# Kernel tuning notes

Measured on AMD Instinct MI355X. Metric: run time of the kernel, lower is better.

The kernel has to match this reference:

```python
import math
import jax, jax.numpy as jnp
import numpy as np

B, N, D = 16384, 16, 2
HIDDEN, DL = 64, 5
OMEGA = 1.0
CUSP_GAMMA = 1.0 / (D - 1)  # dim=2 -> 1.0


def _linear_params(key, fan_in, fan_out):
    kw, kb = jax.random.split(key)
    bound = 1.0 / math.sqrt(fan_in)
    w = jax.random.uniform(kw, (fan_out, fan_in), jnp.float32, -bound, bound)
    b = jax.random.uniform(kb, (fan_out,), jnp.float32, -bound, bound)
    return w, b


def setup_inputs() -> dict:
    key = jax.random.key(0)
    ks = jax.random.split(key, 9)
    x = jax.random.normal(ks[0], (B, N, D), jnp.float32)
    phi_w0, phi_b0 = _linear_params(ks[1], D + 1, HIDDEN)
    phi_w1, phi_b1 = _linear_params(ks[2], HIDDEN, HIDDEN)
    phi_w2, phi_b2 = _linear_params(ks[3], HIDDEN, DL)
    psi_w0, psi_b0 = _linear_params(ks[4], 6, HIDDEN)
    psi_w1, psi_b1 = _linear_params(ks[5], HIDDEN, HIDDEN)
    psi_w2, psi_b2 = _linear_params(ks[6], HIDDEN, DL)
    rho_w0, rho_b0 = _linear_params(ks[7], 2 * DL, HIDDEN)
    # rho output layer: weight std=0.01 normal, bias zeros (matches torch init)
    rho_w1 = 0.01 * jax.random.normal(ks[8], (1, HIDDEN), jnp.float32)
    rho_b1 = jnp.zeros((1,), jnp.float32)
    return dict(x=x,
                phi_w0=phi_w0, phi_b0=phi_b0, phi_w1=phi_w1, phi_b1=phi_b1,
                phi_w2=phi_w2, phi_b2=phi_b2,
                psi_w0=psi_w0, psi_b0=psi_b0, psi_w1=psi_w1, psi_b1=psi_b1,
                psi_w2=psi_w2, psi_b2=psi_b2,
                rho_w0=rho_w0, rho_b0=rho_b0, rho_w1=rho_w1, rho_b1=rho_b1)


def _mlp3(h, w0, b0, w1, b1, w2, b2):
    h = jax.nn.gelu(h @ w0.T + b0, approximate=False)
    h = jax.nn.gelu(h @ w1.T + b1, approximate=False)
    return h @ w2.T + b2


def reference(x, phi_w0, phi_b0, phi_w1, phi_b1, phi_w2, phi_b2,
              psi_w0, psi_b0, psi_w1, psi_b1, psi_w2, psi_b2,
              rho_w0, rho_b0, rho_w1, rho_b1):
    # one-body branch
    xs = x * math.sqrt(OMEGA)                       # [B,N,D]
    r2 = (xs ** 2).sum(-1, keepdims=True)           # [B,N,1]
    phi_in = jnp.concatenate([xs, r2], -1)          # [B,N,D+1]
    phi_out = _mlp3(phi_in, phi_w0, phi_b0, phi_w1, phi_b1, phi_w2, phi_b2).mean(1)  # [B,dL]

    # two-body branch: vectorized over all N*(N-1)/2 pairs
    ii, jj = jnp.triu_indices(N, k=1)               # static pair index lists, P entries
    dr = x[:, ii, :] - x[:, jj, :]                  # [B,P,D]
    rij = jnp.sqrt((dr ** 2).sum(-1) + 1e-12)       # [B,P]
    feat = jnp.stack([jnp.log1p(rij), rij / (1 + rij), jnp.exp(-rij ** 2),
                      jnp.exp(-0.5 * rij), jnp.exp(-rij), jnp.exp(-2 * rij)], -1)  # [B,P,6]
    psi_out = _mlp3(feat, psi_w0, psi_b0, psi_w1, psi_b1, psi_w2, psi_b2).mean(1)  # [B,dL]
    cusp = CUSP_GAMMA * (rij * jnp.exp(-rij)).sum(-1)  # [B]

    # readout
    rho_in = jnp.concatenate([phi_out, psi_out], -1)   # [B,2*dL]
    h = jax.nn.gelu(rho_in @ rho_w0.T + rho_b0, approximate=False)
    f = (h @ rho_w1.T + rho_b1).squeeze(-1)            # [B]
    return f + cusp
```

## Files before the change

### kernel.cpp

```cpp
#include <hip/hip_runtime.h>
#include <hip/hip_bf16.h>
#include <math.h>

#define B_TOT 16384
#define NPART 16
#define NPAIR 120
#define HID   64
#define DL    5
#define GB    4
#define PSI_ROWS 120
#define PHI_HROW 120
#define NROW_IT  136
#define SF_PHI   480

typedef __attribute__((ext_vector_type(8))) short short8;
typedef __attribute__((ext_vector_type(4))) float floatx4;
typedef __attribute__((ext_vector_type(2))) unsigned uintx2;

#define CSC      2.45556851f
#define INV_CSC  0.40723744f

__device__ __forceinline__ float gelu_pre(float z) {
    float e = __builtin_amdgcn_exp2f(-z);
    return z * __builtin_amdgcn_rcpf(1.0f + e);
}

__device__ __forceinline__ float gelu_sig(float v) {
    float e = __builtin_amdgcn_exp2f(-2.45556851f * v);
    return v * __builtin_amdgcn_rcpf(1.0f + e);
}

__device__ __forceinline__ unsigned pk2(float a, float b) {
    __hip_bfloat162 h = __float22bfloat162_rn(make_float2(a, b));
    union { __hip_bfloat162 h; unsigned u; } cv; cv.h = h;
    return cv.u;
}

__device__ __forceinline__ float wred(float v) {
    v += __shfl_down(v, 32);
    v += __shfl_down(v, 16);
    v += __shfl_down(v, 8);
    v += __shfl_down(v, 4);
    v += __shfl_down(v, 2);
    v += __shfl_down(v, 1);
    return v;
}

__global__ __launch_bounds__(256) void jastrow_mfma12(
    const float* __restrict__ x,
    const float* __restrict__ phi_w0, const float* __restrict__ phi_b0,
    const float* __restrict__ phi_w1, const float* __restrict__ phi_b1,
    const float* __restrict__ phi_w2, const float* __restrict__ phi_b2,
    const float* __restrict__ psi_w0, const float* __restrict__ psi_b0,
    const float* __restrict__ psi_w1, const float* __restrict__ psi_b1,
    const float* __restrict__ psi_w2, const float* __restrict__ psi_b2,
    const float* __restrict__ rho_w0, const float* __restrict__ rho_b0,
    const float* __restrict__ rho_w1, const float* __restrict__ rho_b1,
    float* __restrict__ out)
{
    const int t    = threadIdx.x;
    const int lane = t & 63;
    const int wv   = t >> 6;
    const int q    = lane >> 4;
    const int m15  = lane & 15;
    const int bg   = blockIdx.x * GB;

    __shared__ __align__(16) unsigned short s_h[NROW_IT * 64];
    __shared__ __align__(16) unsigned char  s_mem[8704];
    __shared__ float s_cusp[GB];

    unsigned short* s_f  = (unsigned short*)s_mem;
    float*          s_cs = (float*)s_mem;

    const float2* x2 = (const float2*)x;
    float cusp = 0.f;

    {
        const int bl = wv;
        {
            int p = lane;
            int u = 119 - p;
            float sq = sqrtf((float)(8 * u + 1));
            int k = (int)((sq - 1.0f) * 0.5f);
            int i = 14 - k;
            int j = p - (i * (31 - i)) / 2 + i + 1;

            float2 xi = x2[(bg + bl) * NPART + i];
            float2 xj = x2[(bg + bl) * NPART + j];
            float dx = xi.x - xj.x, dy = xi.y - xj.y;
            float r = sqrtf(dx * dx + dy * dy + 1e-12f);

            float f0 = 0.69314718056f * __builtin_amdgcn_logf(1.f + r);
            float f1 = r * __builtin_amdgcn_rcpf(1.f + r);
            float f3 = __builtin_amdgcn_exp2f(-0.72134752044f * r);
            float f4 = f3 * f3;
            float f5 = f4 * f4;
            float f2 = __builtin_amdgcn_exp2f(-1.44269504089f * r * r);
            cusp += r * f4;

            union { short8 s; unsigned u4[4]; } v;
            v.u4[0] = pk2(f0, f1);
            v.u4[1] = pk2(f2, f3);
            v.u4[2] = pk2(f4, f5);
            v.u4[3] = 0u;
            *(short8*)&s_f[(bl * PSI_ROWS + p) * 8] = v.s;
        }
        if (lane < NPAIR - 64) {
            int p = 64 + lane;
            int u = 119 - p;
            float sq = sqrtf((float)(8 * u + 1));
            int k = (int)((sq - 1.0f) * 0.5f);
            int i = 14 - k;
            int j = p - (i * (31 - i)) / 2 + i + 1;

            float2 xi = x2[(bg + bl) * NPART + i];
            float2 xj = x2[(bg + bl) * NPART + j];
            float dx = xi.x - xj.x, dy = xi.y - xj.y;
            float r = sqrtf(dx * dx + dy * dy + 1e-12f);

            float f0 = 0.69314718056f * __builtin_amdgcn_logf(1.f + r);
            float f1 = r * __builtin_amdgcn_rcpf(1.f + r);
            float f3 = __builtin_amdgcn_exp2f(-0.72134752044f * r);
            float f4 = f3 * f3;
            float f5 = f4 * f4;
            float f2 = __builtin_amdgcn_exp2f(-1.44269504089f * r * r);
            cusp += r * f4;

            union { short8 s; unsigned u4[4]; } v;
            v.u4[0] = pk2(f0, f1);
            v.u4[1] = pk2(f2, f3);
            v.u4[2] = pk2(f4, f5);
            v.u4[3] = 0u;
            *(short8*)&s_f[(bl * PSI_ROWS + p) * 8] = v.s;
        }
        if (lane >= 48) {
            int n = lane - 48;
            float2 xv = x2[(bg + bl) * NPART + n];
            float r2 = xv.x * xv.x + xv.y * xv.y;
            union { short8 s; unsigned u4[4]; } w;
            w.u4[0] = pk2(xv.x, xv.y);
            w.u4[1] = pk2(r2, 0.f);
            w.u4[2] = 0u; w.u4[3] = 0u;
            *(short8*)&s_f[(SF_PHI + bl * NPART + n) * 8] = w.s;
        }
    }

    const int colb = wv * 16 + m15;

    short8 Ap1[4];
    floatx4 C0p4[4];
#pragma unroll
    for (int ht = 0; ht < 4; ++ht) {
        short8 f = (short8)0;
        if (q == 0) {
            const float* w = psi_w0 + (ht * 16 + m15) * 6;
            union { short8 s; unsigned u4[4]; } bb;
            bb.u4[0] = pk2(CSC * w[0], CSC * w[1]);
            bb.u4[1] = pk2(CSC * w[2], CSC * w[3]);
            bb.u4[2] = pk2(CSC * w[4], CSC * w[5]);
            bb.u4[3] = 0u;
            f = bb.s;
        }
        Ap1[ht] = f;
        floatx4 bv = *(const floatx4*)(psi_b0 + ht * 16 + q * 4);
        C0p4[ht] = bv * CSC;
    }
    short8 Af1 = (short8)0;
    if (q == 0) {
        const float* wf = phi_w0 + (wv * 16 + m15) * 3;
        union { short8 s; unsigned u4[4]; } bb;
        bb.u4[0] = pk2(CSC * wf[0], CSC * wf[1]);
        bb.u4[1] = pk2(CSC * wf[2], 0.f);
        bb.u4[2] = 0u; bb.u4[3] = 0u;
        Af1 = bb.s;
    }
    floatx4 C0fv = (*(const floatx4*)(phi_b0 + wv * 16 + q * 4)) * CSC;

    int scolw[4];
#pragma unroll
    for (int ht = 0; ht < 4; ++ht)
        scolw[ht] = (ht * 16 + q * 4) ^ ((m15 & 7) << 3);
    const int scolwp = (wv * 16 + q * 4) ^ ((m15 & 7) << 3);

    short8 Bp2[2], Bf2[2];
#pragma unroll
    for (int Kc = 0; Kc < 2; ++Kc) {
        const floatx4* wp4 = (const floatx4*)(psi_w1 + colb * HID + Kc * 32 + q * 8);
        const floatx4* wf4 = (const floatx4*)(phi_w1 + colb * HID + Kc * 32 + q * 8);
        floatx4 pA = wp4[0], pB = wp4[1];
        floatx4 fA = wf4[0], fB = wf4[1];
        union { short8 s; unsigned u4[4]; } bp, bf;
        bp.u4[0] = pk2(pA[0], pA[1]); bp.u4[1] = pk2(pA[2], pA[3]);
        bp.u4[2] = pk2(pB[0], pB[1]); bp.u4[3] = pk2(pB[2], pB[3]);
        bf.u4[0] = pk2(fA[0], fA[1]); bf.u4[1] = pk2(fA[2], fA[3]);
        bf.u4[2] = pk2(fB[0], fB[1]); bf.u4[3] = pk2(fB[2], fB[3]);
        Bp2[Kc] = bp.s; Bf2[Kc] = bf.s;
    }
    float b1p = CSC * psi_b1[colb], b1f = CSC * phi_b1[colb];
    floatx4 C1p = {b1p, b1p, b1p, b1p};
    floatx4 C1f = {b1f, b1f, b1f, b1f};

    const int g0 = ((q ^ (m15 & 7)) << 3);
    const int g1 = g0 ^ 32;

    float csP[GB] = {0.f, 0.f, 0.f, 0.f};
    float csF[GB] = {0.f, 0.f, 0.f, 0.f};

    __syncthreads();

#pragma unroll
    for (int bl = 0; bl < GB; ++bl) {
#pragma unroll
        for (int ti = 0; ti < 2; ++ti) {
            const int Mt = wv * 2 + ti;
            short8 b = *(const short8*)&s_f[(bl * PSI_ROWS + Mt * 16 + m15) * 8];
            unsigned short* wp = &s_h[(Mt * 16 + m15) * 64];
            const bool wr = (Mt != 7) || (m15 < 8);
#pragma unroll
            for (int ht = 0; ht < 4; ++ht) {
                floatx4 d = __builtin_amdgcn_mfma_f32_16x16x32_bf16(Ap1[ht], b, C0p4[ht], 0, 0, 0);
                unsigned u0 = pk2(gelu_pre(d[0]), gelu_pre(d[1]));
                unsigned u1 = pk2(gelu_pre(d[2]), gelu_pre(d[3]));
                if (wr) {
                    uintx2 v = {u0, u1};
                    *(uintx2*)(wp + scolw[ht]) = v;
                }
            }
        }
        {
            short8 b = *(const short8*)&s_f[(SF_PHI + bl * NPART + m15) * 8];
            unsigned short* wp = &s_h[(PHI_HROW + m15) * 64];
            floatx4 d = __builtin_amdgcn_mfma_f32_16x16x32_bf16(Af1, b, C0fv, 0, 0, 0);
            unsigned u0 = pk2(gelu_pre(d[0]), gelu_pre(d[1]));
            unsigned u1 = pk2(gelu_pre(d[2]), gelu_pre(d[3]));
            uintx2 v = {u0, u1};
            *(uintx2*)(wp + scolwp) = v;
        }
        __syncthreads();

#pragma unroll
        for (int Mt = 0; Mt < 8; ++Mt) {
            int rb = (Mt * 16 + m15) * 64;
            short8 a0 = *(const short8*)&s_h[rb + g0];
            short8 a1 = *(const short8*)&s_h[rb + g1];
            floatx4 acc = __builtin_amdgcn_mfma_f32_16x16x32_bf16(a0, Bp2[0], C1p, 0, 0, 0);
            acc = __builtin_amdgcn_mfma_f32_16x16x32_bf16(a1, Bp2[1], acc, 0, 0, 0);
            if (Mt == 7) {
                if (q < 2) {
#pragma unroll
                    for (int rg = 0; rg < 4; ++rg) {
                        float z = acc[rg];
                        float rr = __builtin_amdgcn_rcpf(1.0f + __builtin_amdgcn_exp2f(-z));
                        csP[bl] = __builtin_fmaf(z, rr, csP[bl]);
                    }
                }
            } else {
#pragma unroll
                for (int rg = 0; rg < 4; ++rg) {
                    float z = acc[rg];
                    float rr = __builtin_amdgcn_rcpf(1.0f + __builtin_amdgcn_exp2f(-z));
                    csP[bl] = __builtin_fmaf(z, rr, csP[bl]);
                }
            }
        }
        {
            int rb = (PHI_HROW + m15) * 64;
            short8 a0 = *(const short8*)&s_h[rb + g0];
            short8 a1 = *(const short8*)&s_h[rb + g1];
            floatx4 acc = __builtin_amdgcn_mfma_f32_16x16x32_bf16(a0, Bf2[0], C1f, 0, 0, 0);
            acc = __builtin_amdgcn_mfma_f32_16x16x32_bf16(a1, Bf2[1], acc, 0, 0, 0);
#pragma unroll
            for (int rg = 0; rg < 4; ++rg) {
                float z = acc[rg];
                float rr = __builtin_amdgcn_rcpf(1.0f + __builtin_amdgcn_exp2f(-z));
                csF[bl] = __builtin_fmaf(z, rr, csF[bl]);
            }
        }
        if (bl < GB - 1) __syncthreads();
    }

#pragma unroll
    for (int bl = 0; bl < GB; ++bl) {
        s_cs[(((0 * GB + bl) * 4 + wv) * 4 + q) * 16 + m15] = csP[bl];
        s_cs[(((1 * GB + bl) * 4 + wv) * 4 + q) * 16 + m15] = csF[bl];
    }
    {
        float cc = wred(cusp);
        if (lane == 0) s_cusp[wv] = cc;
    }
    __syncthreads();

    {
        const int blr = wv;
        const int c   = lane;
        const int cw  = c >> 4, cm = c & 15;
        float colP = 0.f, colF = 0.f;
#pragma unroll
        for (int qq = 0; qq < 4; ++qq) {
            colP += s_cs[(((0 * GB + blr) * 4 + cw) * 4 + qq) * 16 + cm];
            colF += s_cs[(((1 * GB + blr) * 4 + cw) * 4 + qq) * 16 + cm];
        }
        colP *= INV_CSC;
        colF *= INV_CSC;

        float psiv[DL], phiv[DL];
#pragma unroll
        for (int d = 0; d < DL; ++d) {
            float sP = wred(colP * psi_w2[d * HID + c]);
            psiv[d] = __shfl(sP, 0) * (1.0f / NPAIR) + psi_b2[d];
            float sF = wred(colF * phi_w2[d * HID + c]);
            phiv[d] = __shfl(sF, 0) * (1.0f / NPART) + phi_b2[d];
        }

        int j = lane;
        float a = rho_b0[j];
        const float* wr = rho_w0 + j * (2 * DL);
#pragma unroll
        for (int d = 0; d < DL; ++d)
            a += phiv[d] * wr[d] + psiv[d] * wr[DL + d];
        float cuspb = s_cusp[blr];
        float cv = gelu_sig(a) * rho_w1[j];
        cv = wred(cv);
        if (j == 0) out[bg + blr] = cv + rho_b1[0] + cuspb;
    }
}

extern "C" void kernel_launch(void* const* d_in, const int* in_sizes, int n_in,
                              void* d_out, int out_size, void* d_ws, size_t ws_size,
                              hipStream_t stream) {
    const float* x      = (const float*)d_in[0];
    const float* phi_w0 = (const float*)d_in[1];
    const float* phi_b0 = (const float*)d_in[2];
    const float* phi_w1 = (const float*)d_in[3];
    const float* phi_b1 = (const float*)d_in[4];
    const float* phi_w2 = (const float*)d_in[5];
    const float* phi_b2 = (const float*)d_in[6];
    const float* psi_w0 = (const float*)d_in[7];
    const float* psi_b0 = (const float*)d_in[8];
    const float* psi_w1 = (const float*)d_in[9];
    const float* psi_b1 = (const float*)d_in[10];
    const float* psi_w2 = (const float*)d_in[11];
    const float* psi_b2 = (const float*)d_in[12];
    const float* rho_w0 = (const float*)d_in[13];
    const float* rho_b0 = (const float*)d_in[14];
    const float* rho_w1 = (const float*)d_in[15];
    const float* rho_b1 = (const float*)d_in[16];

    jastrow_mfma12<<<B_TOT / GB, 256, 0, stream>>>(
        x,
        phi_w0, phi_b0, phi_w1, phi_b1, phi_w2, phi_b2,
        psi_w0, psi_b0, psi_w1, psi_b1, psi_w2, psi_b2,
        rho_w0, rho_b0, rho_w1, rho_b1,
        (float*)d_out);
}
```

Measured before the change: 176.9 us.

## Make each wave own one sample and keep MLP hidden activations in registers

Result: slower. 187.6 us (+6.0%).

```diff
diff --git a/kernel.cpp b/kernel.cpp
--- a/kernel.cpp
+++ b/kernel.cpp
@@ -8,17 +8,19 @@
 #define HID   64
 #define DL    5
 #define GB    4
-#define PSI_ROWS 120
-#define PHI_HROW 120
-#define NROW_IT  136
-#define SF_PHI   480
+#define SROWS 136
 
 typedef __attribute__((ext_vector_type(8))) short short8;
 typedef __attribute__((ext_vector_type(4))) float floatx4;
-typedef __attribute__((ext_vector_type(2))) unsigned uintx2;
 
 #define CSC      2.45556851f
 #define INV_CSC  0.40723744f
+
+__device__ __forceinline__ unsigned pk2(float a, float b) {
+    unsigned r;
+    asm("v_cvt_pk_bf16_f32 %0, %1, %2" : "=v"(r) : "v"(a), "v"(b));
+    return r;
+}
 
 __device__ __forceinline__ float gelu_pre(float z) {
     float e = __builtin_amdgcn_exp2f(-z);
@@ -28,12 +30,6 @@
 __device__ __forceinline__ float gelu_sig(float v) {
     float e = __builtin_amdgcn_exp2f(-2.45556851f * v);
     return v * __builtin_amdgcn_rcpf(1.0f + e);
-}
-
-__device__ __forceinline__ unsigned pk2(float a, float b) {
-    __hip_bfloat162 h = __float22bfloat162_rn(make_float2(a, b));
-    union { __hip_bfloat162 h; unsigned u; } cv; cv.h = h;
-    return cv.u;
 }
 
 __device__ __forceinline__ float wred(float v) {
@@ -46,7 +42,11 @@
     return v;
 }
 
-__global__ __launch_bounds__(256) void jastrow_mfma12(
+__device__ __forceinline__ int hperm(int ht, int m) {
+    return ((ht & 1) << 2) + ((ht >> 1) << 5) + ((m >> 2) << 3) + (m & 3);
+}
+
+__global__ __launch_bounds__(256, 4) void jastrow_wave(
     const float* __restrict__ x,
     const float* __restrict__ phi_w0, const float* __restrict__ phi_b0,
     const float* __restrict__ phi_w1, const float* __restrict__ phi_b1,
@@ -65,18 +65,15 @@
     const int m15  = lane & 15;
     const int bg   = blockIdx.x * GB;
 
-    __shared__ __align__(16) unsigned short s_h[NROW_IT * 64];
-    __shared__ __align__(16) unsigned char  s_mem[8704];
-    __shared__ float s_cusp[GB];
-
-    unsigned short* s_f  = (unsigned short*)s_mem;
-    float*          s_cs = (float*)s_mem;
+    __shared__ __align__(16) unsigned short s_f[GB * SROWS * 8];
+    __shared__ float s_cs[GB * 2 * HID];
+    unsigned short* sf = s_f + wv * SROWS * 8;
 
     const float2* x2 = (const float2*)x;
+    const int bi = bg + wv;
     float cusp = 0.f;
 
     {
-        const int bl = wv;
         {
             int p = lane;
             int u = 119 - p;
@@ -85,8 +82,8 @@
             int i = 14 - k;
             int j = p - (i * (31 - i)) / 2 + i + 1;
 
-            float2 xi = x2[(bg + bl) * NPART + i];
-            float2 xj = x2[(bg + bl) * NPART + j];
+            float2 xi = x2[bi * NPART + i];
+            float2 xj = x2[bi * NPART + j];
             float dx = xi.x - xj.x, dy = xi.y - xj.y;
             float r = sqrtf(dx * dx + dy * dy + 1e-12f);
 
@@ -102,8 +99,8 @@
             v.u4[0] = pk2(f0, f1);
             v.u4[1] = pk2(f2, f3);
             v.u4[2] = pk2(f4, f5);
-            v.u4[3] = 0u;
-            *(short8*)&s_f[(bl * PSI_ROWS + p) * 8] = v.s;
+            v.u4[3] = pk2(1.0f, 0.f);
+            *(short8*)&sf[p * 8] = v.s;
         }
         if (lane < NPAIR - 64) {
             int p = 64 + lane;
@@ -113,8 +110,8 @@
             int i = 14 - k;
             int j = p - (i * (31 - i)) / 2 + i + 1;
 
-            float2 xi = x2[(bg + bl) * NPART + i];
-            float2 xj = x2[(bg + bl) * NPART + j];
+            float2 xi = x2[bi * NPART + i];
+            float2 xj = x2[bi * NPART + j];
             float dx = xi.x - xj.x, dy = xi.y - xj.y;
             float r = sqrtf(dx * dx + dy * dy + 1e-12f);
 
@@ -130,178 +127,199 @@
             v.u4[0] = pk2(f0, f1);
             v.u4[1] = pk2(f2, f3);
             v.u4[2] = pk2(f4, f5);
-            v.u4[3] = 0u;
-            *(short8*)&s_f[(bl * PSI_ROWS + p) * 8] = v.s;
+            v.u4[3] = pk2(1.0f, 0.f);
+            *(short8*)&sf[p * 8] = v.s;
         }
         if (lane >= 48) {
             int n = lane - 48;
-            float2 xv = x2[(bg + bl) * NPART + n];
+            float2 xv = x2[bi * NPART + n];
             float r2 = xv.x * xv.x + xv.y * xv.y;
             union { short8 s; unsigned u4[4]; } w;
             w.u4[0] = pk2(xv.x, xv.y);
-            w.u4[1] = pk2(r2, 0.f);
+            w.u4[1] = pk2(r2, 1.0f);
             w.u4[2] = 0u; w.u4[3] = 0u;
-            *(short8*)&s_f[(SF_PHI + bl * NPART + n) * 8] = w.s;
-        }
-    }
-
-    const int colb = wv * 16 + m15;
-
-    short8 Ap1[4];
-    floatx4 C0p4[4];
+            *(short8*)&sf[(120 + n) * 8] = w.s;
+        }
+    }
+    float cusp_b;
+    { float cc = wred(cusp); cusp_b = __shfl(cc, 0); }
+
+    const floatx4 zf4 = {0.f, 0.f, 0.f, 0.f};
+
+    short8 A1p[4];
 #pragma unroll
     for (int ht = 0; ht < 4; ++ht) {
         short8 f = (short8)0;
         if (q == 0) {
-            const float* w = psi_w0 + (ht * 16 + m15) * 6;
+            int h = hperm(ht, m15);
+            const float* w = psi_w0 + h * 6;
             union { short8 s; unsigned u4[4]; } bb;
             bb.u4[0] = pk2(CSC * w[0], CSC * w[1]);
             bb.u4[1] = pk2(CSC * w[2], CSC * w[3]);
             bb.u4[2] = pk2(CSC * w[4], CSC * w[5]);
-            bb.u4[3] = 0u;
+            bb.u4[3] = pk2(CSC * psi_b0[h], 0.f);
             f = bb.s;
         }
-        Ap1[ht] = f;
-        floatx4 bv = *(const floatx4*)(psi_b0 + ht * 16 + q * 4);
-        C0p4[ht] = bv * CSC;
-    }
-    short8 Af1 = (short8)0;
-    if (q == 0) {
-        const float* wf = phi_w0 + (wv * 16 + m15) * 3;
-        union { short8 s; unsigned u4[4]; } bb;
-        bb.u4[0] = pk2(CSC * wf[0], CSC * wf[1]);
-        bb.u4[1] = pk2(CSC * wf[2], 0.f);
-        bb.u4[2] = 0u; bb.u4[3] = 0u;
-        Af1 = bb.s;
-    }
-    floatx4 C0fv = (*(const floatx4*)(phi_b0 + wv * 16 + q * 4)) * CSC;
-
-    int scolw[4];
-#pragma unroll
-    for (int ht = 0; ht < 4; ++ht)
-        scolw[ht] = (ht * 16 + q * 4) ^ ((m15 & 7) << 3);
-    const int scolwp = (wv * 16 + q * 4) ^ ((m15 & 7) << 3);
-
-    short8 Bp2[2], Bf2[2];
-#pragma unroll
-    for (int Kc = 0; Kc < 2; ++Kc) {
-        const floatx4* wp4 = (const floatx4*)(psi_w1 + colb * HID + Kc * 32 + q * 8);
-        const floatx4* wf4 = (const floatx4*)(phi_w1 + colb * HID + Kc * 32 + q * 8);
-        floatx4 pA = wp4[0], pB = wp4[1];
-        floatx4 fA = wf4[0], fB = wf4[1];
-        union { short8 s; unsigned u4[4]; } bp, bf;
-        bp.u4[0] = pk2(pA[0], pA[1]); bp.u4[1] = pk2(pA[2], pA[3]);
-        bp.u4[2] = pk2(pB[0], pB[1]); bp.u4[3] = pk2(pB[2], pB[3]);
-        bf.u4[0] = pk2(fA[0], fA[1]); bf.u4[1] = pk2(fA[2], fA[3]);
-        bf.u4[2] = pk2(fB[0], fB[1]); bf.u4[3] = pk2(fB[2], fB[3]);
-        Bp2[Kc] = bp.s; Bf2[Kc] = bf.s;
-    }
-    float b1p = CSC * psi_b1[colb], b1f = CSC * phi_b1[colb];
-    floatx4 C1p = {b1p, b1p, b1p, b1p};
-    floatx4 C1f = {b1f, b1f, b1f, b1f};
-
-    const int g0 = ((q ^ (m15 & 7)) << 3);
-    const int g1 = g0 ^ 32;
-
-    float csP[GB] = {0.f, 0.f, 0.f, 0.f};
-    float csF[GB] = {0.f, 0.f, 0.f, 0.f};
-
-    __syncthreads();
-
-#pragma unroll
-    for (int bl = 0; bl < GB; ++bl) {
-#pragma unroll
-        for (int ti = 0; ti < 2; ++ti) {
-            const int Mt = wv * 2 + ti;
-            short8 b = *(const short8*)&s_f[(bl * PSI_ROWS + Mt * 16 + m15) * 8];
-            unsigned short* wp = &s_h[(Mt * 16 + m15) * 64];
-            const bool wr = (Mt != 7) || (m15 < 8);
-#pragma unroll
-            for (int ht = 0; ht < 4; ++ht) {
-                floatx4 d = __builtin_amdgcn_mfma_f32_16x16x32_bf16(Ap1[ht], b, C0p4[ht], 0, 0, 0);
-                unsigned u0 = pk2(gelu_pre(d[0]), gelu_pre(d[1]));
-                unsigned u1 = pk2(gelu_pre(d[2]), gelu_pre(d[3]));
-                if (wr) {
-                    uintx2 v = {u0, u1};
-                    *(uintx2*)(wp + scolw[ht]) = v;
-                }
-            }
-        }
-        {
-            short8 b = *(const short8*)&s_f[(SF_PHI + bl * NPART + m15) * 8];
-            unsigned short* wp = &s_h[(PHI_HROW + m15) * 64];
-            floatx4 d = __builtin_amdgcn_mfma_f32_16x16x32_bf16(Af1, b, C0fv, 0, 0, 0);
-            unsigned u0 = pk2(gelu_pre(d[0]), gelu_pre(d[1]));
-            unsigned u1 = pk2(gelu_pre(d[2]), gelu_pre(d[3]));
-            uintx2 v = {u0, u1};
-            *(uintx2*)(wp + scolwp) = v;
-        }
-        __syncthreads();
-
-#pragma unroll
-        for (int Mt = 0; Mt < 8; ++Mt) {
-            int rb = (Mt * 16 + m15) * 64;
-            short8 a0 = *(const short8*)&s_h[rb + g0];
-            short8 a1 = *(const short8*)&s_h[rb + g1];
-            floatx4 acc = __builtin_amdgcn_mfma_f32_16x16x32_bf16(a0, Bp2[0], C1p, 0, 0, 0);
-            acc = __builtin_amdgcn_mfma_f32_16x16x32_bf16(a1, Bp2[1], acc, 0, 0, 0);
-            if (Mt == 7) {
-                if (q < 2) {
-#pragma unroll
-                    for (int rg = 0; rg < 4; ++rg) {
-                        float z = acc[rg];
-                        float rr = __builtin_amdgcn_rcpf(1.0f + __builtin_amdgcn_exp2f(-z));
-                        csP[bl] = __builtin_fmaf(z, rr, csP[bl]);
-                    }
-                }
-            } else {
-#pragma unroll
-                for (int rg = 0; rg < 4; ++rg) {
-                    float z = acc[rg];
-                    float rr = __builtin_amdgcn_rcpf(1.0f + __builtin_amdgcn_exp2f(-z));
-                    csP[bl] = __builtin_fmaf(z, rr, csP[bl]);
-                }
-            }
-        }
-        {
-            int rb = (PHI_HROW + m15) * 64;
-            short8 a0 = *(const short8*)&s_h[rb + g0];
-            short8 a1 = *(const short8*)&s_h[rb + g1];
-            floatx4 acc = __builtin_amdgcn_mfma_f32_16x16x32_bf16(a0, Bf2[0], C1f, 0, 0, 0);
-            acc = __builtin_amdgcn_mfma_f32_16x16x32_bf16(a1, Bf2[1], acc, 0, 0, 0);
+        A1p[ht] = f;
+    }
+    short8 A2p[4][2];
+    floatx4 C1p[4];
+#pragma unroll
+    for (int ht2 = 0; ht2 < 4; ++ht2) {
+        int h2 = hperm(ht2, m15);
+#pragma unroll
+        for (int ks = 0; ks < 2; ++ks) {
+            const floatx4* wp = (const floatx4*)(psi_w1 + h2 * HID + ks * 32 + q * 8);
+            floatx4 wa = wp[0], wb = wp[1];
+            union { short8 s; unsigned u4[4]; } bb;
+            bb.u4[0] = pk2(wa[0], wa[1]); bb.u4[1] = pk2(wa[2], wa[3]);
+            bb.u4[2] = pk2(wb[0], wb[1]); bb.u4[3] = pk2(wb[2], wb[3]);
+            A2p[ht2][ks] = bb.s;
+        }
+        int cb = ((ht2 & 1) << 2) + ((ht2 >> 1) << 5) + (q << 3);
+        floatx4 bv = *(const floatx4*)(psi_b1 + cb);
+        C1p[ht2] = bv * CSC;
+    }
+
+    float CS[16];
+#pragma unroll
+    for (int i = 0; i < 16; ++i) CS[i] = 0.f;
+
+#pragma unroll
+    for (int Mt = 0; Mt < 8; ++Mt) {
+        short8 b = *(const short8*)&sf[(Mt * 16 + m15) * 8];
+        floatx4 d0 = __builtin_amdgcn_mfma_f32_16x16x32_bf16(A1p[0], b, zf4, 0, 0, 0);
+        floatx4 d1 = __builtin_amdgcn_mfma_f32_16x16x32_bf16(A1p[1], b, zf4, 0, 0, 0);
+        union { short8 s; unsigned u4[4]; } Bk0, Bk1;
+        Bk0.u4[0] = pk2(gelu_pre(d0[0]), gelu_pre(d0[1]));
+        Bk0.u4[1] = pk2(gelu_pre(d0[2]), gelu_pre(d0[3]));
+        Bk0.u4[2] = pk2(gelu_pre(d1[0]), gelu_pre(d1[1]));
+        Bk0.u4[3] = pk2(gelu_pre(d1[2]), gelu_pre(d1[3]));
+        floatx4 d2 = __builtin_amdgcn_mfma_f32_16x16x32_bf16(A1p[2], b, zf4, 0, 0, 0);
+        floatx4 d3 = __builtin_amdgcn_mfma_f32_16x16x32_bf16(A1p[3], b, zf4, 0, 0, 0);
+        Bk1.u4[0] = pk2(gelu_pre(d2[0]), gelu_pre(d2[1]));
+        Bk1.u4[1] = pk2(gelu_pre(d2[2]), gelu_pre(d2[3]));
+        Bk1.u4[2] = pk2(gelu_pre(d3[0]), gelu_pre(d3[1]));
+        Bk1.u4[3] = pk2(gelu_pre(d3[2]), gelu_pre(d3[3]));
+
+#pragma unroll
+        for (int ht2 = 0; ht2 < 4; ++ht2) {
+            floatx4 acc = __builtin_amdgcn_mfma_f32_16x16x32_bf16(A2p[ht2][0], Bk0.s, C1p[ht2], 0, 0, 0);
+            acc = __builtin_amdgcn_mfma_f32_16x16x32_bf16(A2p[ht2][1], Bk1.s, acc, 0, 0, 0);
 #pragma unroll
             for (int rg = 0; rg < 4; ++rg) {
                 float z = acc[rg];
                 float rr = __builtin_amdgcn_rcpf(1.0f + __builtin_amdgcn_exp2f(-z));
-                csF[bl] = __builtin_fmaf(z, rr, csF[bl]);
-            }
-        }
-        if (bl < GB - 1) __syncthreads();
-    }
-
-#pragma unroll
-    for (int bl = 0; bl < GB; ++bl) {
-        s_cs[(((0 * GB + bl) * 4 + wv) * 4 + q) * 16 + m15] = csP[bl];
-        s_cs[(((1 * GB + bl) * 4 + wv) * 4 + q) * 16 + m15] = csF[bl];
-    }
+                if (Mt == 7) {
+                    float p = z * rr;
+                    p = (m15 < 8) ? p : 0.f;
+                    CS[ht2 * 4 + rg] += p;
+                } else {
+                    CS[ht2 * 4 + rg] = __builtin_fmaf(z, rr, CS[ht2 * 4 + rg]);
+                }
+            }
+        }
+    }
+
+#pragma unroll
+    for (int i = 0; i < 16; ++i) {
+        CS[i] += __shfl_xor(CS[i], 1);
+        CS[i] += __shfl_xor(CS[i], 2);
+        CS[i] += __shfl_xor(CS[i], 4);
+        CS[i] += __shfl_xor(CS[i], 8);
+    }
+#pragma unroll
+    for (int i = 0; i < 16; ++i) {
+        if (m15 == i) {
+            int h2 = ((i >> 2) & 1) * 4 + (i >> 3) * 32 + q * 8 + (i & 3);
+            s_cs[(wv * 2 + 0) * HID + h2] = CS[i];
+        }
+    }
+
+    __builtin_amdgcn_sched_barrier(0);
+
     {
-        float cc = wred(cusp);
-        if (lane == 0) s_cusp[wv] = cc;
-    }
-    __syncthreads();
+        short8 A1f[4];
+#pragma unroll
+        for (int ht = 0; ht < 4; ++ht) {
+            short8 f = (short8)0;
+            if (q == 0) {
+                int h = hperm(ht, m15);
+                const float* w = phi_w0 + h * 3;
+                union { short8 s; unsigned u4[4]; } bb;
+                bb.u4[0] = pk2(CSC * w[0], CSC * w[1]);
+                bb.u4[1] = pk2(CSC * w[2], CSC * phi_b0[h]);
+                bb.u4[2] = 0u; bb.u4[3] = 0u;
+                f = bb.s;
+            }
+            A1f[ht] = f;
+        }
+        short8 A2f[4][2];
+        floatx4 C1f[4];
+#pragma unroll
+        for (int ht2 = 0; ht2 < 4; ++ht2) {
+            int h2 = hperm(ht2, m15);
+#pragma unroll
+            for (int ks = 0; ks < 2; ++ks) {
+                const floatx4* wp = (const floatx4*)(phi_w1 + h2 * HID + ks * 32 + q * 8);
+                floatx4 wa = wp[0], wb = wp[1];
+                union { short8 s; unsigned u4[4]; } bb;
+                bb.u4[0] = pk2(wa[0], wa[1]); bb.u4[1] = pk2(wa[2], wa[3]);
+                bb.u4[2] = pk2(wb[0], wb[1]); bb.u4[3] = pk2(wb[2], wb[3]);
+                A2f[ht2][ks] = bb.s;
+            }
+            int cb = ((ht2 & 1) << 2) + ((ht2 >> 1) << 5) + (q << 3);
+            floatx4 bv = *(const floatx4*)(phi_b1 + cb);
+            C1f[ht2] = bv * CSC;
+        }
+
+        float CF[16];
+        short8 b = *(const short8*)&sf[(120 + m15) * 8];
+        floatx4 d0 = __builtin_amdgcn_mfma_f32_16x16x32_bf16(A1f[0], b, zf4, 0, 0, 0);
+        floatx4 d1 = __builtin_amdgcn_mfma_f32_16x16x32_bf16(A1f[1], b, zf4, 0, 0, 0);
+        union { short8 s; unsigned u4[4]; } Bk0, Bk1;
+        Bk0.u4[0] = pk2(gelu_pre(d0[0]), gelu_pre(d0[1]));
+        Bk0.u4[1] = pk2(gelu_pre(d0[2]), gelu_pre(d0[3]));
+        Bk0.u4[2] = pk2(gelu_pre(d1[0]), gelu_pre(d1[1]));
+        Bk0.u4[3] = pk2(gelu_pre(d1[2]), gelu_pre(d1[3]));
+        floatx4 d2 = __builtin_amdgcn_mfma_f32_16x16x32_bf16(A1f[2], b, zf4, 0, 0, 0);
+        floatx4 d3 = __builtin_amdgcn_mfma_f32_16x16x32_bf16(A1f[3], b, zf4, 0, 0, 0);
+        Bk1.u4[0] = pk2(gelu_pre(d2[0]), gelu_pre(d2[1]));
+        Bk1.u4[1] = pk2(gelu_pre(d2[2]), gelu_pre(d2[3]));
+        Bk1.u4[2] = pk2(gelu_pre(d3[0]), gelu_pre(d3[1]));
+        Bk1.u4[3] = pk2(gelu_pre(d3[2]), gelu_pre(d3[3]));
+
+#pragma unroll
+        for (int ht2 = 0; ht2 < 4; ++ht2) {
+            floatx4 acc = __builtin_amdgcn_mfma_f32_16x16x32_bf16(A2f[ht2][0], Bk0.s, C1f[ht2], 0, 0, 0);
+            acc = __builtin_amdgcn_mfma_f32_16x16x32_bf16(A2f[ht2][1], Bk1.s, acc, 0, 0, 0);
+#pragma unroll
+            for (int rg = 0; rg < 4; ++rg) {
+                float z = acc[rg];
+                float rr = __builtin_amdgcn_rcpf(1.0f + __builtin_amdgcn_exp2f(-z));
+                CF[ht2 * 4 + rg] = z * rr;
+            }
+        }
+#pragma unroll
+        for (int i = 0; i < 16; ++i) {
+            CF[i] += __shfl_xor(CF[i], 1);
+            CF[i] += __shfl_xor(CF[i], 2);
+            CF[i] += __shfl_xor(CF[i], 4);
+            CF[i] += __shfl_xor(CF[i], 8);
+        }
+#pragma unroll
+        for (int i = 0; i < 16; ++i) {
+            if (m15 == i) {
+                int h2 = ((i >> 2) & 1) * 4 + (i >> 3) * 32 + q * 8 + (i & 3);
+                s_cs[(wv * 2 + 1) * HID + h2] = CF[i];
+            }
+        }
+    }
 
     {
-        const int blr = wv;
-        const int c   = lane;
-        const int cw  = c >> 4, cm = c & 15;
-        float colP = 0.f, colF = 0.f;
-#pragma unroll
-        for (int qq = 0; qq < 4; ++qq) {
-            colP += s_cs[(((0 * GB + blr) * 4 + cw) * 4 + qq) * 16 + cm];
-            colF += s_cs[(((1 * GB + blr) * 4 + cw) * 4 + qq) * 16 + cm];
-        }
-        colP *= INV_CSC;
-        colF *= INV_CSC;
+        const int c = lane;
+        float colP = s_cs[(wv * 2 + 0) * HID + c] * INV_CSC;
+        float colF = s_cs[(wv * 2 + 1) * HID + c] * INV_CSC;
 
         float psiv[DL], phiv[DL];
 #pragma unroll
@@ -318,10 +336,9 @@
 #pragma unroll
         for (int d = 0; d < DL; ++d)
             a += phiv[d] * wr[d] + psiv[d] * wr[DL + d];
-        float cuspb = s_cusp[blr];
         float cv = gelu_sig(a) * rho_w1[j];
         cv = wred(cv);
-        if (j == 0) out[bg + blr] = cv + rho_b1[0] + cuspb;
+        if (j == 0) out[bi] = cv + rho_b1[0] + cusp_b;
     }
 }
 
@@ -346,7 +363,7 @@
     const float* rho_w1 = (const float*)d_in[15];
     const float* rho_b1 = (const float*)d_in[16];
 
-    jastrow_mfma12<<<B_TOT / GB, 256, 0, stream>>>(
+    jastrow_wave<<<B_TOT / GB, 256, 0, stream>>>(
         x,
         phi_w0, phi_b0, phi_w1, phi_b1, phi_w2, phi_b2,
         psi_w0, psi_b0, psi_w1, psi_b1, psi_w2, psi_b2,
```
